# Optimization experiments

Measured on AMD Instinct MI355X. Metric: run time of the kernel, lower is better.

The kernel has to match this reference:

```python
import jax, jax.numpy as jnp
import numpy as np

GROUPS = 32
EPS = 1e-5   # nn.GroupNorm default


def group_norm(x, gamma, beta):
    # x: [B, C, H, W]
    b, c, h, w = x.shape
    xg = x.reshape(b, GROUPS, c // GROUPS, h, w)
    mu = jnp.mean(xg, axis=(2, 3, 4), keepdims=True)
    var = jnp.var(xg, axis=(2, 3, 4), keepdims=True)
    xn = ((xg - mu) * jax.lax.rsqrt(var + EPS)).reshape(b, c, h, w)
    return xn * gamma[None, :, None, None] + beta[None, :, None, None]


def conv1x1(x, w, b):
    # x: [B, C, H, W], w: [O, C], b: [O]
    return jnp.einsum('bchw,oc->bohw', x, w) + b[None, :, None, None]


def setup_inputs() -> dict:
    key = jax.random.key(0)
    ks = jax.random.split(key, 10)
    B, C, H, W = 8, 512, 64, 64
    std = 1.0 / np.sqrt(C)
    inp = {
        'x': jax.random.normal(ks[0], (B, C, H, W), dtype=jnp.float32),
        'gn_gamma': jnp.ones((C,), dtype=jnp.float32),
        'gn_beta': jnp.zeros((C,), dtype=jnp.float32),
        'wq': jax.random.normal(ks[1], (C, C), dtype=jnp.float32) * std,
        'bq': jnp.zeros((C,), dtype=jnp.float32),
        'wk': jax.random.normal(ks[2], (C, C), dtype=jnp.float32) * std,
        'bk': jnp.zeros((C,), dtype=jnp.float32),
        'wv': jax.random.normal(ks[3], (C, C), dtype=jnp.float32) * std,
        'bv': jnp.zeros((C,), dtype=jnp.float32),
        'wp': jax.random.normal(ks[4], (C, C), dtype=jnp.float32) * std,
        'bp': jnp.zeros((C,), dtype=jnp.float32),
    }
    return inp


def reference(x, gn_gamma, gn_beta, wq, bq, wk, bk, wv, bv, wp, bp):
    b, c, hh, ww = x.shape
    n = hh * ww
    h = group_norm(x, gn_gamma, gn_beta)
    q = conv1x1(h, wq, bq).reshape(b, c, n).transpose(0, 2, 1)  # [B, N, C]
    k = conv1x1(h, wk, bk).reshape(b, c, n)                     # [B, C, N]
    v = conv1x1(h, wv, bv).reshape(b, c, n).transpose(0, 2, 1)  # [B, N, C]
    scale = 1.0 / jnp.sqrt(jnp.asarray(c, dtype=x.dtype))
    attn = jax.nn.softmax(jnp.einsum('bnc,bcm->bnm', q, k) * scale, axis=-1)
    out = jnp.einsum('bnm,bmc->bnc', attn, v)                   # [B, N, C]
    out = out.transpose(0, 2, 1).reshape(b, c, hh, ww)
    return x + conv1x1(out, wp, bp)
```

## Files before the change

kernel.cpp:

```cpp
#include <hip/hip_runtime.h>


typedef __attribute__((ext_vector_type(8))) __bf16 bf16x8;
typedef __attribute__((ext_vector_type(4))) __bf16 bf16x4;
typedef __attribute__((ext_vector_type(4))) float f32x4;
typedef unsigned int u32;

#define DEVICE __device__ __forceinline__

DEVICE void async_copy16(const void* g, void* l) {
  __builtin_amdgcn_global_load_lds(
      (__attribute__((address_space(1))) u32*)(g),
      (__attribute__((address_space(3))) u32*)(l),
      16, 0, 0);
}

__global__ __launch_bounds__(256) void cvt_w(
    const float* __restrict__ w0, const float* __restrict__ w1,
    const float* __restrict__ w2, const float* __restrict__ w3,
    __bf16* __restrict__ o0, __bf16* __restrict__ o1,
    __bf16* __restrict__ o2, __bf16* __restrict__ o3) {
  int idx = blockIdx.x * 256 + threadIdx.x;
  int off = idx * 8;
  int m = off >> 18;
  int r = off & 262143;
  const float* src = m == 0 ? w0 : m == 1 ? w1 : m == 2 ? w2 : w3;
  __bf16* dst = m == 0 ? o0 : m == 1 ? o1 : m == 2 ? o2 : o3;
  float4 a = *(const float4*)(src + r);
  float4 b = *(const float4*)(src + r + 4);
  bf16x8 v = {(__bf16)a.x, (__bf16)a.y, (__bf16)a.z, (__bf16)a.w,
              (__bf16)b.x, (__bf16)b.y, (__bf16)b.z, (__bf16)b.w};
  *(bf16x8*)(dst + r) = v;
}

__global__ __launch_bounds__(256) void gn_stats(const float* __restrict__ x,
                                                float* __restrict__ stats) {
  int bg = blockIdx.x;
  const float* p = x + (size_t)bg * 65536;
  int t = threadIdx.x, lane = t & 63, w = t >> 6;
  float s = 0.f, ss = 0.f;
  for (int i = t; i < 16384; i += 256) {
    float4 v = *(const float4*)(p + i * 4);
    s += v.x + v.y + v.z + v.w;
    ss += v.x * v.x + v.y * v.y + v.z * v.z + v.w * v.w;
  }
#pragma unroll
  for (int off = 32; off; off >>= 1) {
    s += __shfl_xor(s, off);
    ss += __shfl_xor(ss, off);
  }
  __shared__ float rs_[4], rss_[4];
  if (lane == 0) { rs_[w] = s; rss_[w] = ss; }
  __syncthreads();
  if (t == 0) {
    float S = rs_[0] + rs_[1] + rs_[2] + rs_[3];
    float SS = rss_[0] + rss_[1] + rss_[2] + rss_[3];
    float mean = S * (1.0f / 65536.0f);
    float var = SS * (1.0f / 65536.0f) - mean * mean;
    stats[bg * 2] = mean;
    stats[bg * 2 + 1] = rsqrtf(var + 1e-5f);
  }
}

__global__ __launch_bounds__(256) void gn_apply(
    const float* __restrict__ x, const float* __restrict__ gamma,
    const float* __restrict__ beta, const float* __restrict__ stats,
    __bf16* __restrict__ h) {
  int b = blockIdx.z, g = blockIdx.y;
  int n = blockIdx.x * 256 + threadIdx.x;
  const float* px = x + ((size_t)b * 512 + g * 16) * 4096 + n;
  float mean = stats[(b * 32 + g) * 2];
  float rstd = stats[(b * 32 + g) * 2 + 1];
  bf16x8 lo, hi;
#pragma unroll
  for (int c = 0; c < 8; ++c) {
    float v = px[(size_t)c * 4096];
    lo[c] = (__bf16)((v - mean) * rstd * gamma[g * 16 + c] + beta[g * 16 + c]);
  }
#pragma unroll
  for (int c = 0; c < 8; ++c) {
    float v = px[(size_t)(c + 8) * 4096];
    hi[c] = (__bf16)((v - mean) * rstd * gamma[g * 16 + c + 8] + beta[g * 16 + c + 8]);
  }
  __bf16* dst = h + ((size_t)b * 4096 + n) * 512 + g * 16;
  *(bf16x8*)dst = lo;
  *(bf16x8*)(dst + 8) = hi;
}

template <int EPI>
__global__ __launch_bounds__(256) void gemm_bt(
    const __bf16* __restrict__ A, const __bf16* __restrict__ B,
    void* __restrict__ Cout, int K, int lda, int ldb, int ldc,
    const float* __restrict__ bias, const float* __restrict__ resid,
    long sA, long sB, long sC, long sR) {
  int z = blockIdx.z;
  A += (size_t)z * sA;
  B += (size_t)z * sB;
  __shared__ __bf16 lA[128 * 32];
  __shared__ __bf16 lB[128 * 32];
  int t = threadIdx.x, lane = t & 63, w = t >> 6;
  int row0 = blockIdx.x * 128, col0 = blockIdx.y * 128;
  int wr = w >> 1, wc = w & 1;
  f32x4 acc[4][4] = {};

  int sw = ((lane & 15) >> 1) & 3;
  int ca = ((lane >> 4) ^ sw) << 3;

  for (int k0 = 0; k0 < K; k0 += 32) {
    __syncthreads();
#pragma unroll
    for (int r = 0; r < 2; ++r) {
      int chunk = r * 256 + w * 64 + lane;
      int row = chunk >> 2;
      int csrc = ((chunk & 3) ^ ((row >> 1) & 3)) << 3;
      async_copy16(A + (size_t)(row0 + row) * lda + k0 + csrc,
                   lA + (r * 256 + w * 64) * 8);
    }
#pragma unroll
    for (int r = 0; r < 2; ++r) {
      int chunk = r * 256 + w * 64 + lane;
      int row = chunk >> 2;
      int csrc = ((chunk & 3) ^ ((row >> 1) & 3)) << 3;
      async_copy16(B + (size_t)(col0 + row) * ldb + k0 + csrc,
                   lB + (r * 256 + w * 64) * 8);
    }
    __syncthreads();
    bf16x8 af[4], bf[4];
#pragma unroll
    for (int i = 0; i < 4; ++i) {
      af[i] = *(const bf16x8*)(lA + (wr * 64 + i * 16 + (lane & 15)) * 32 + ca);
      bf[i] = *(const bf16x8*)(lB + (wc * 64 + i * 16 + (lane & 15)) * 32 + ca);
    }
#pragma unroll
    for (int i = 0; i < 4; ++i)
#pragma unroll
      for (int j = 0; j < 4; ++j)
        acc[i][j] = __builtin_amdgcn_mfma_f32_16x16x32_bf16(af[i], bf[j], acc[i][j], 0, 0, 0);
  }

  int rbase = row0 + wr * 64, cbase = col0 + wc * 64;
#pragma unroll
  for (int i = 0; i < 4; ++i) {
#pragma unroll
    for (int j = 0; j < 4; ++j) {
      int col = cbase + j * 16 + (lane & 15);
#pragma unroll
      for (int rg = 0; rg < 4; ++rg) {
        int row = rbase + i * 16 + (lane >> 4) * 4 + rg;
        float v = acc[i][j][rg];
        size_t idx = (size_t)z * sC + (size_t)row * ldc + col;
        if constexpr (EPI == 0) {
          ((__bf16*)Cout)[idx] = (__bf16)(v + bias[col]);
        } else if constexpr (EPI == 1) {
          ((__bf16*)Cout)[idx] = (__bf16)(v + bias[row]);
        } else {
          ((float*)Cout)[idx] =
              v + bias[row] + resid[(size_t)z * sR + (size_t)row * ldc + col];
        }
      }
    }
  }
}


#define G256_PHASE(BUF, QR, QC, RDA, RDB, STAGE_STMT, TAIL_STMT)               \
  do {                                                                         \
    if (RDA) {                                                                 \
      _Pragma("unroll") for (int fr = 0; fr < 4; ++fr) {                       \
        a[fr][0] = ldA(BUF, (QR)*4 + fr, 0);                                   \
        a[fr][1] = ldA(BUF, (QR)*4 + fr, 1);                                   \
      }                                                                        \
    }                                                                          \
    if (RDB) {                                                                 \
      _Pragma("unroll") for (int fc = 0; fc < 2; ++fc) {                       \
        b[(QC)*2 + fc][0] = ldB(BUF, (QC)*2 + fc, 0);                          \
        b[(QC)*2 + fc][1] = ldB(BUF, (QC)*2 + fc, 1);                          \
      }                                                                        \
    }                                                                          \
    STAGE_STMT;                                                                \
    __builtin_amdgcn_s_barrier();                                              \
    asm volatile("s_waitcnt lgkmcnt(0)" ::: "memory");                         \
    __builtin_amdgcn_sched_barrier(0);                                         \
    __builtin_amdgcn_s_setprio(1);                                             \
    _Pragma("unroll") for (int fr = 0; fr < 4; ++fr)                           \
      _Pragma("unroll") for (int fc = 0; fc < 2; ++fc) {                       \
        acc[(QR)*4 + fr][(QC)*2 + fc] =                                        \
            __builtin_amdgcn_mfma_f32_16x16x32_bf16(                           \
                a[fr][0], b[(QC)*2 + fc][0], acc[(QR)*4 + fr][(QC)*2 + fc],    \
                0, 0, 0);                                                      \
        acc[(QR)*4 + fr][(QC)*2 + fc] =                                        \
            __builtin_amdgcn_mfma_f32_16x16x32_bf16(                           \
                a[fr][1], b[(QC)*2 + fc][1], acc[(QR)*4 + fr][(QC)*2 + fc],    \
                0, 0, 0);                                                      \
      }                                                                        \
    __builtin_amdgcn_s_setprio(0);                                             \
    TAIL_STMT;                                                                 \
    __builtin_amdgcn_sched_barrier(0);                                         \
    __builtin_amdgcn_s_barrier();                                              \
  } while (0)

#define G256_ITER(T0, T1, LAST)                                                \
  G256_PHASE(0, 0, 0, 1, 1, stage(1, 0, 0, (T1)), ((void)0));                  \
  G256_PHASE(0, 0, 1, 0, 1, stage(1, 0, 1, (T1)), ((void)0));                  \
  G256_PHASE(0, 1, 0, 1, 0,                                                    \
             if (!(LAST)) stage(0, 1, 0, (T0) + 2), ((void)0));                \
  G256_PHASE(0, 1, 1, 0, 0,                                                    \
             if (!(LAST)) stage(0, 1, 1, (T0) + 2),                            \
             if (LAST) {                                                       \
               asm volatile("s_waitcnt vmcnt(0)" ::: "memory");                \
             } else {                                                          \
               asm volatile("s_waitcnt vmcnt(4)" ::: "memory");                \
             });                                                               \
  G256_PHASE(1, 0, 0, 1, 1,                                                    \
             if (!(LAST)) stage(0, 0, 0, (T0) + 2), ((void)0));                \
  G256_PHASE(1, 0, 1, 0, 1,                                                    \
             if (!(LAST)) stage(0, 0, 1, (T0) + 2), ((void)0));                \
  G256_PHASE(1, 1, 0, 1, 0,                                                    \
             if (!(LAST)) stage(1, 1, 0, (T1) + 2), ((void)0));                \
  G256_PHASE(1, 1, 1, 0, 0,                                                    \
             if (!(LAST)) stage(1, 1, 1, (T1) + 2),                            \
             if (!(LAST)) {                                                    \
               asm volatile("s_waitcnt vmcnt(4)" ::: "memory");                \
             })

__global__ __launch_bounds__(512, 2) void gemm256(
    const __bf16* __restrict__ A, const __bf16* __restrict__ B,
    __bf16* __restrict__ Cout, int lda, int ldb, int ldc, int nIter, int nTM,
    int nTN, int KS, long sA, long sKA, long sB, long sKB, long sC) {
  __shared__ __bf16 lds_raw[2][2][2][128][64];

  int nwg = gridDim.x, bid = blockIdx.x;
  int qq = nwg >> 3, rr = nwg & 7;
  int xcd = bid & 7, ii = bid >> 3;
  int swz = (xcd < rr ? xcd * (qq + 1) : rr * (qq + 1) + (xcd - rr) * qq) + ii;
  int tn = swz % nTN;
  int tm = (swz / nTN) % nTM;
  int zz = swz / (nTN * nTM);
  int z = zz / KS, ks = zz % KS;
  A += (size_t)z * sA + (size_t)ks * sKA;
  B += (size_t)z * sB + (size_t)ks * sKB;
  Cout += (size_t)zz * sC;
  int row0 = tm * 256, col0 = tn * 256;

  int tid = threadIdx.x;
  int wid = tid >> 6, lane = tid & 63;
  int wr = wid >> 2, wc = wid & 3;
  int l15 = lane & 15, l4 = lane >> 4;

  auto stage = [&](int buf, int mat, int half, int kt) {
    const __bf16* src = mat ? B : A;
    int ld = mat ? ldb : lda;
    int rbase = (mat ? col0 : row0) + half * 128;
    char* ldsbase =
        (char*)lds_raw + (((buf * 2 + mat) * 2 + half) * 16384);
#pragma unroll
    for (int L = 0; L < 2; ++L) {
      int ci = L * 512 + tid;
      int r = ci >> 3, cslot = ci & 7;
      int csrc = cslot ^ (r & 7);
      async_copy16(src + (size_t)(rbase + r) * ld + kt * 64 + csrc * 8,
                   ldsbase + (L * 512 + wid * 64) * 16);
    }
  };
  auto ldA = [&](int buf, int fr, int kh) -> bf16x8 {
    int row = fr * 16 + l15;
    int g = kh * 4 + l4;
    char* base = (char*)lds_raw + (((buf * 2 + 0) * 2 + wr) * 16384);
    return *(const bf16x8*)(base + row * 128 + ((g ^ (row & 7)) * 16));
  };
  auto ldB = [&](int buf, int fc, int kh) -> bf16x8 {
    int row = (wc & 1) * 64 + fc * 16 + l15;
    int g = kh * 4 + l4;
    char* base = (char*)lds_raw + (((buf * 2 + 1) * 2 + (wc >> 1)) * 16384);
    return *(const bf16x8*)(base + row * 128 + ((g ^ (row & 7)) * 16));
  };

  f32x4 acc[8][4] = {};
  bf16x8 a[4][2], b[4][2];

  stage(0, 1, 0, 0);
  stage(0, 1, 1, 0);
  stage(0, 0, 0, 0);
  stage(0, 0, 1, 0);
  stage(1, 1, 0, 1);
  stage(1, 1, 1, 1);
  asm volatile("s_waitcnt vmcnt(4)" ::: "memory");
  __builtin_amdgcn_sched_barrier(0);
  __builtin_amdgcn_s_barrier();

  int it = 0;
  for (; it < nIter - 1; ++it) {
    G256_ITER(2 * it, 2 * it + 1, 0);
  }
  G256_ITER(2 * it, 2 * it + 1, 1);

  int rb = row0 + wr * 128, cb = col0 + wc * 64;
#pragma unroll
  for (int fr = 0; fr < 8; ++fr) {
#pragma unroll
    for (int fc = 0; fc < 4; ++fc) {
      int col = cb + fc * 16 + l15;
#pragma unroll
      for (int rg = 0; rg < 4; ++rg) {
        int row = rb + fr * 16 + l4 * 4 + rg;
        Cout[(size_t)row * ldc + col] = (__bf16)acc[fr][fc][rg];
      }
    }
  }
}

__global__ __launch_bounds__(256) void softmax_rows_bf16(__bf16* __restrict__ S) {
  int row = blockIdx.x;
  __bf16* p = S + (size_t)row * 4096;
  int t = threadIdx.x, lane = t & 63, w = t >> 6;
  const float c1 = 0.04419417382415922f * 1.4426950408889634f;
  bf16x8 v0 = *(const bf16x8*)(p + t * 16);
  bf16x8 v1 = *(const bf16x8*)(p + t * 16 + 8);
  float f[16];
  float mx = -3.4e38f;
#pragma unroll
  for (int i = 0; i < 8; ++i) { f[i] = (float)v0[i]; mx = fmaxf(mx, f[i]); }
#pragma unroll
  for (int i = 0; i < 8; ++i) { f[8 + i] = (float)v1[i]; mx = fmaxf(mx, f[8 + i]); }
#pragma unroll
  for (int off = 32; off; off >>= 1) mx = fmaxf(mx, __shfl_xor(mx, off));
  __shared__ float rm[4], rsum[4];
  if (lane == 0) rm[w] = mx;
  __syncthreads();
  float m = fmaxf(fmaxf(rm[0], rm[1]), fmaxf(rm[2], rm[3]));
  float s = 0.f;
#pragma unroll
  for (int i = 0; i < 16; ++i) {
    f[i] = exp2f((f[i] - m) * c1);
    s += f[i];
  }
#pragma unroll
  for (int off = 32; off; off >>= 1) s += __shfl_xor(s, off);
  if (lane == 0) rsum[w] = s;
  __syncthreads();
  float inv = 1.0f / (rsum[0] + rsum[1] + rsum[2] + rsum[3]);
  bf16x8 o0, o1;
#pragma unroll
  for (int i = 0; i < 8; ++i) o0[i] = (__bf16)(f[i] * inv);
#pragma unroll
  for (int i = 0; i < 8; ++i) o1[i] = (__bf16)(f[8 + i] * inv);
  *(bf16x8*)(p + t * 16) = o0;
  *(bf16x8*)(p + t * 16 + 8) = o1;
}

__global__ __launch_bounds__(256) void reduce4(const __bf16* __restrict__ part,
                                               __bf16* __restrict__ out) {
  int z = blockIdx.y;
  size_t e = ((size_t)blockIdx.x * 256 + threadIdx.x) * 8;
  const __bf16* p = part + (size_t)z * 4 * 2097152 + e;
  bf16x8 v0 = *(const bf16x8*)(p);
  bf16x8 v1 = *(const bf16x8*)(p + 2097152);
  bf16x8 v2 = *(const bf16x8*)(p + 2 * 2097152);
  bf16x8 v3 = *(const bf16x8*)(p + 3 * 2097152);
  bf16x8 o;
#pragma unroll
  for (int j = 0; j < 8; ++j)
    o[j] = (__bf16)((float)v0[j] + (float)v1[j] + (float)v2[j] + (float)v3[j]);
  *(bf16x8*)(out + (size_t)z * 2097152 + e) = o;
}

extern "C" void kernel_launch(void* const* d_in, const int* in_sizes, int n_in,
                              void* d_out, int out_size, void* d_ws, size_t ws_size,
                              hipStream_t stream) {
  const float* x = (const float*)d_in[0];
  const float* gamma = (const float*)d_in[1];
  const float* beta = (const float*)d_in[2];
  const float* wq = (const float*)d_in[3];
  const float* bq = (const float*)d_in[4];
  const float* wk = (const float*)d_in[5];
  const float* bk = (const float*)d_in[6];
  const float* wv = (const float*)d_in[7];
  const float* bv = (const float*)d_in[8];
  const float* wp = (const float*)d_in[9];
  const float* bp = (const float*)d_in[10];

  char* p = (char*)d_ws;
  auto alloc = [&](size_t bytes) {
    char* r = p;
    p += (bytes + 255) & ~(size_t)255;
    return r;
  };
  float* stats = (float*)alloc(256 * 2 * 4);
  __bf16* wqb = (__bf16*)alloc(512 * 512 * 2);
  __bf16* wkb = (__bf16*)alloc(512 * 512 * 2);
  __bf16* wvb = (__bf16*)alloc(512 * 512 * 2);
  __bf16* wpb = (__bf16*)alloc(512 * 512 * 2);
  __bf16* ho = (__bf16*)alloc((size_t)8 * 4096 * 512 * 2);
  __bf16* q = (__bf16*)alloc((size_t)8 * 4096 * 512 * 2);
  __bf16* kb = (__bf16*)alloc((size_t)8 * 4096 * 512 * 2);
  __bf16* vt = (__bf16*)alloc((size_t)8 * 512 * 4096 * 2);

  const size_t SB = (size_t)4096 * 4096 * 2;
  const size_t PB = (size_t)4 * 4096 * 512 * 2;
  size_t used = (size_t)(p - (char*)d_ws);
  size_t freeb = (ws_size > used) ? ws_size - used : 0;
  int nb = (int)(freeb / (SB + PB));
  if (nb > 8) nb = 8;
  if (nb < 1) nb = 1;
  __bf16* s = (__bf16*)alloc(SB * nb);
  __bf16* pvp = (__bf16*)alloc(PB * nb);

  cvt_w<<<512, 256, 0, stream>>>(wq, wk, wv, wp, wqb, wkb, wvb, wpb);
  gn_stats<<<256, 256, 0, stream>>>(x, stats);
  gn_apply<<<dim3(16, 32, 8), 256, 0, stream>>>(x, gamma, beta, stats, ho);

  gemm_bt<0><<<dim3(256, 4, 1), 256, 0, stream>>>(ho, wqb, q, 512, 512, 512, 512,
                                                  bq, nullptr, 0, 0, 0, 0);
  gemm_bt<0><<<dim3(256, 4, 1), 256, 0, stream>>>(ho, wkb, kb, 512, 512, 512, 512,
                                                  bk, nullptr, 0, 0, 0, 0);
  gemm_bt<1><<<dim3(4, 32, 8), 256, 0, stream>>>(wvb, ho, vt, 512, 512, 512, 4096,
                                                 bv, nullptr, 0, 2097152, 2097152, 0);

  __bf16* o = ho;
  for (int b0 = 0; b0 < 8; b0 += nb) {
    int zb = (8 - b0 < nb) ? (8 - b0) : nb;
    gemm256<<<dim3(zb * 256), 512, 0, stream>>>(
        q + (size_t)b0 * 2097152, kb + (size_t)b0 * 2097152, s, 512, 512, 4096,
        4, 16, 16, 1, 2097152, 0, 2097152, 0, 16777216);
    softmax_rows_bf16<<<zb * 4096, 256, 0, stream>>>(s);
    gemm256<<<dim3(zb * 4 * 32), 512, 0, stream>>>(
        s, vt + (size_t)b0 * 2097152, pvp, 4096, 4096, 512, 8, 16, 2, 4,
        16777216, 1024, 2097152, 1024, 2097152);
    reduce4<<<dim3(1024, zb), 256, 0, stream>>>(pvp, o + (size_t)b0 * 2097152);
  }
  gemm_bt<3><<<dim3(4, 32, 8), 256, 0, stream>>>(
      wpb, o, d_out, 512, 512, 512, 4096, bp, x, 0, 2097152, 2097152, 2097152);
}
```

Measured before the change: 639.8 us.

## Fuse Q/K projections and route all projections through the pipelined 256-tile GEMM

Concatenates the Q and K weights so a single GEMM produces an interleaved QK buffer. The V and output projections move from the simple 128-tile gemm_bt kernel to the templated, double-buffered gemm256 kernel with bias and residual epilogues. The output projection writes NCHW float4 stores with the residual added directly. This is meant to cut launches and raise MFMA efficiency on the projection GEMMs, at the cost of strided QK reads (ld 1024) in the attention GEMM and a more complex epilogue.

```diff
diff --git a/kernel.cpp b/kernel.cpp
--- a/kernel.cpp
+++ b/kernel.cpp
@@ -2,7 +2,6 @@
 
 
 typedef __attribute__((ext_vector_type(8))) __bf16 bf16x8;
-typedef __attribute__((ext_vector_type(4))) __bf16 bf16x4;
 typedef __attribute__((ext_vector_type(4))) float f32x4;
 typedef unsigned int u32;
 
@@ -85,81 +84,6 @@
   __bf16* dst = h + ((size_t)b * 4096 + n) * 512 + g * 16;
   *(bf16x8*)dst = lo;
   *(bf16x8*)(dst + 8) = hi;
-}
-
-template <int EPI>
-__global__ __launch_bounds__(256) void gemm_bt(
-    const __bf16* __restrict__ A, const __bf16* __restrict__ B,
-    void* __restrict__ Cout, int K, int lda, int ldb, int ldc,
-    const float* __restrict__ bias, const float* __restrict__ resid,
-    long sA, long sB, long sC, long sR) {
-  int z = blockIdx.z;
-  A += (size_t)z * sA;
-  B += (size_t)z * sB;
-  __shared__ __bf16 lA[128 * 32];
-  __shared__ __bf16 lB[128 * 32];
-  int t = threadIdx.x, lane = t & 63, w = t >> 6;
-  int row0 = blockIdx.x * 128, col0 = blockIdx.y * 128;
-  int wr = w >> 1, wc = w & 1;
-  f32x4 acc[4][4] = {};
-
-  int sw = ((lane & 15) >> 1) & 3;
-  int ca = ((lane >> 4) ^ sw) << 3;
-
-  for (int k0 = 0; k0 < K; k0 += 32) {
-    __syncthreads();
-#pragma unroll
-    for (int r = 0; r < 2; ++r) {
-      int chunk = r * 256 + w * 64 + lane;
-      int row = chunk >> 2;
-      int csrc = ((chunk & 3) ^ ((row >> 1) & 3)) << 3;
-      async_copy16(A + (size_t)(row0 + row) * lda + k0 + csrc,
-                   lA + (r * 256 + w * 64) * 8);
-    }
-#pragma unroll
-    for (int r = 0; r < 2; ++r) {
-      int chunk = r * 256 + w * 64 + lane;
-      int row = chunk >> 2;
-      int csrc = ((chunk & 3) ^ ((row >> 1) & 3)) << 3;
-      async_copy16(B + (size_t)(col0 + row) * ldb + k0 + csrc,
-                   lB + (r * 256 + w * 64) * 8);
-    }
-    __syncthreads();
-    bf16x8 af[4], bf[4];
-#pragma unroll
-    for (int i = 0; i < 4; ++i) {
-      af[i] = *(const bf16x8*)(lA + (wr * 64 + i * 16 + (lane & 15)) * 32 + ca);
-      bf[i] = *(const bf16x8*)(lB + (wc * 64 + i * 16 + (lane & 15)) * 32 + ca);
-    }
-#pragma unroll
-    for (int i = 0; i < 4; ++i)
-#pragma unroll
-      for (int j = 0; j < 4; ++j)
-        acc[i][j] = __builtin_amdgcn_mfma_f32_16x16x32_bf16(af[i], bf[j], acc[i][j], 0, 0, 0);
-  }
-
-  int rbase = row0 + wr * 64, cbase = col0 + wc * 64;
-#pragma unroll
-  for (int i = 0; i < 4; ++i) {
-#pragma unroll
-    for (int j = 0; j < 4; ++j) {
-      int col = cbase + j * 16 + (lane & 15);
-#pragma unroll
-      for (int rg = 0; rg < 4; ++rg) {
-        int row = rbase + i * 16 + (lane >> 4) * 4 + rg;
-        float v = acc[i][j][rg];
-        size_t idx = (size_t)z * sC + (size_t)row * ldc + col;
-        if constexpr (EPI == 0) {
-          ((__bf16*)Cout)[idx] = (__bf16)(v + bias[col]);
-        } else if constexpr (EPI == 1) {
-          ((__bf16*)Cout)[idx] = (__bf16)(v + bias[row]);
-        } else {
-          ((float*)Cout)[idx] =
-              v + bias[row] + resid[(size_t)z * sR + (size_t)row * ldc + col];
-        }
-      }
-    }
-  }
 }
 
 
@@ -223,10 +147,13 @@
                asm volatile("s_waitcnt vmcnt(4)" ::: "memory");                \
              })
 
+template <int EPI>
 __global__ __launch_bounds__(512, 2) void gemm256(
     const __bf16* __restrict__ A, const __bf16* __restrict__ B,
-    __bf16* __restrict__ Cout, int lda, int ldb, int ldc, int nIter, int nTM,
-    int nTN, int KS, long sA, long sKA, long sB, long sKB, long sC) {
+    void* __restrict__ CoutV, int lda, int ldb, int ldc, int nIter, int nTM,
+    int nTN, int KS, long sA, long sKA, long sB, long sKB, long sC,
+    const float* __restrict__ bias0, const float* __restrict__ bias1,
+    const float* __restrict__ resid) {
   __shared__ __bf16 lds_raw[2][2][2][128][64];
 
   int nwg = gridDim.x, bid = blockIdx.x;
@@ -239,7 +166,7 @@
   int z = zz / KS, ks = zz % KS;
   A += (size_t)z * sA + (size_t)ks * sKA;
   B += (size_t)z * sB + (size_t)ks * sKB;
-  Cout += (size_t)zz * sC;
+  __bf16* Cout = (__bf16*)CoutV + (size_t)zz * sC;
   int row0 = tm * 256, col0 = tn * 256;
 
   int tid = threadIdx.x;
@@ -251,8 +178,7 @@
     const __bf16* src = mat ? B : A;
     int ld = mat ? ldb : lda;
     int rbase = (mat ? col0 : row0) + half * 128;
-    char* ldsbase =
-        (char*)lds_raw + (((buf * 2 + mat) * 2 + half) * 16384);
+    char* ldsbase = (char*)lds_raw + (((buf * 2 + mat) * 2 + half) * 16384);
 #pragma unroll
     for (int L = 0; L < 2; ++L) {
       int ci = L * 512 + tid;
@@ -300,10 +226,26 @@
 #pragma unroll
     for (int fc = 0; fc < 4; ++fc) {
       int col = cb + fc * 16 + l15;
-#pragma unroll
-      for (int rg = 0; rg < 4; ++rg) {
-        int row = rb + fr * 16 + l4 * 4 + rg;
-        Cout[(size_t)row * ldc + col] = (__bf16)acc[fr][fc][rg];
+      if constexpr (EPI == 3) {
+        int r0 = rb + fr * 16 + l4 * 4;
+        size_t idx = ((size_t)(r0 >> 12) * 512 + col) * 4096 + (r0 & 4095);
+        float4 rv = *(const float4*)(resid + idx);
+        float bb = bias0[col];
+        float4 ov = {acc[fr][fc][0] + bb + rv.x, acc[fr][fc][1] + bb + rv.y,
+                     acc[fr][fc][2] + bb + rv.z, acc[fr][fc][3] + bb + rv.w};
+        *(float4*)((float*)CoutV + idx) = ov;
+      } else {
+        float cbias = 0.f;
+        if constexpr (EPI == 1)
+          cbias = col < 512 ? bias0[col] : bias1[col - 512];
+#pragma unroll
+        for (int rg = 0; rg < 4; ++rg) {
+          int row = rb + fr * 16 + l4 * 4 + rg;
+          float v = acc[fr][fc][rg];
+          if constexpr (EPI == 1) v += cbias;
+          if constexpr (EPI == 2) v += bias0[row];
+          Cout[(size_t)row * ldc + col] = (__bf16)v;
+        }
       }
     }
   }
@@ -386,13 +328,11 @@
     return r;
   };
   float* stats = (float*)alloc(256 * 2 * 4);
-  __bf16* wqb = (__bf16*)alloc(512 * 512 * 2);
-  __bf16* wkb = (__bf16*)alloc(512 * 512 * 2);
+  __bf16* wqkb = (__bf16*)alloc((size_t)1024 * 512 * 2);
   __bf16* wvb = (__bf16*)alloc(512 * 512 * 2);
   __bf16* wpb = (__bf16*)alloc(512 * 512 * 2);
   __bf16* ho = (__bf16*)alloc((size_t)8 * 4096 * 512 * 2);
-  __bf16* q = (__bf16*)alloc((size_t)8 * 4096 * 512 * 2);
-  __bf16* kb = (__bf16*)alloc((size_t)8 * 4096 * 512 * 2);
+  __bf16* qk = (__bf16*)alloc((size_t)8 * 4096 * 1024 * 2);
   __bf16* vt = (__bf16*)alloc((size_t)8 * 512 * 4096 * 2);
 
   const size_t SB = (size_t)4096 * 4096 * 2;
@@ -405,29 +345,29 @@
   __bf16* s = (__bf16*)alloc(SB * nb);
   __bf16* pvp = (__bf16*)alloc(PB * nb);
 
-  cvt_w<<<512, 256, 0, stream>>>(wq, wk, wv, wp, wqb, wkb, wvb, wpb);
+  cvt_w<<<512, 256, 0, stream>>>(wq, wk, wv, wp, wqkb, wqkb + 262144, wvb, wpb);
   gn_stats<<<256, 256, 0, stream>>>(x, stats);
   gn_apply<<<dim3(16, 32, 8), 256, 0, stream>>>(x, gamma, beta, stats, ho);
 
-  gemm_bt<0><<<dim3(256, 4, 1), 256, 0, stream>>>(ho, wqb, q, 512, 512, 512, 512,
-                                                  bq, nullptr, 0, 0, 0, 0);
-  gemm_bt<0><<<dim3(256, 4, 1), 256, 0, stream>>>(ho, wkb, kb, 512, 512, 512, 512,
-                                                  bk, nullptr, 0, 0, 0, 0);
-  gemm_bt<1><<<dim3(4, 32, 8), 256, 0, stream>>>(wvb, ho, vt, 512, 512, 512, 4096,
-                                                 bv, nullptr, 0, 2097152, 2097152, 0);
+  gemm256<1><<<dim3(512), 512, 0, stream>>>(
+      ho, wqkb, qk, 512, 512, 1024, 4, 128, 4, 1, 0, 0, 0, 0, 0, bq, bk, nullptr);
+  gemm256<2><<<dim3(256), 512, 0, stream>>>(
+      wvb, ho, vt, 512, 512, 4096, 4, 2, 16, 1, 0, 0, 2097152, 0, 2097152,
+      bv, nullptr, nullptr);
 
   __bf16* o = ho;
   for (int b0 = 0; b0 < 8; b0 += nb) {
     int zb = (8 - b0 < nb) ? (8 - b0) : nb;
-    gemm256<<<dim3(zb * 256), 512, 0, stream>>>(
-        q + (size_t)b0 * 2097152, kb + (size_t)b0 * 2097152, s, 512, 512, 4096,
-        4, 16, 16, 1, 2097152, 0, 2097152, 0, 16777216);
+    gemm256<0><<<dim3(zb * 256), 512, 0, stream>>>(
+        qk + (size_t)b0 * 4194304, qk + (size_t)b0 * 4194304 + 512, s, 1024,
+        1024, 4096, 4, 16, 16, 1, 4194304, 0, 4194304, 0, 16777216,
+        nullptr, nullptr, nullptr);
     softmax_rows_bf16<<<zb * 4096, 256, 0, stream>>>(s);
-    gemm256<<<dim3(zb * 4 * 32), 512, 0, stream>>>(
+    gemm256<0><<<dim3(zb * 128), 512, 0, stream>>>(
         s, vt + (size_t)b0 * 2097152, pvp, 4096, 4096, 512, 8, 16, 2, 4,
-        16777216, 1024, 2097152, 1024, 2097152);
+        16777216, 1024, 2097152, 1024, 2097152, nullptr, nullptr, nullptr);
     reduce4<<<dim3(1024, zb), 256, 0, stream>>>(pvp, o + (size_t)b0 * 2097152);
   }
-  gemm_bt<3><<<dim3(4, 32, 8), 256, 0, stream>>>(
-      wpb, o, d_out, 512, 512, 512, 4096, bp, x, 0, 2097152, 2097152, 2097152);
-}
+  gemm256<3><<<dim3(256), 512, 0, stream>>>(
+      o, wpb, d_out, 512, 512, 0, 4, 128, 2, 1, 0, 0, 0, 0, 0, bp, nullptr, x);
+}
```

New measurement: 609.7 us. 4.7% less time.
